# Kernel optimization log

Measured on AMD Instinct MI355X. Metric: run time of the kernel, lower is better.

## Reference

```python
import jax, jax.numpy as jnp
import numpy as np

EPS = 1e-5

def rms_norm(x):
    # SimpleRMSNorm (no learned weight), as used inside BitLinear158
    return x * jax.lax.rsqrt(jnp.mean(x * x, axis=-1, keepdims=True) + EPS)

def act_quant(x):
    # int8 absmax quantization per last-dim row, with straight-through estimator
    scale = 127.0 / jnp.clip(jnp.max(jnp.abs(x), axis=-1, keepdims=True), 1e-5)
    q = jnp.clip(jnp.round(x * scale), -128.0, 127.0) / scale
    return x + jax.lax.stop_gradient(q - x)

def weight_quant(w):
    # ternary {-1,0,1} absmean quantization, with straight-through estimator
    scale = 1.0 / jnp.clip(jnp.mean(jnp.abs(w)), 1e-5)
    q = jnp.clip(jnp.round(w * scale), -1.0, 1.0) / scale
    return w + jax.lax.stop_gradient(q - w)

def bitlinear158(x, w, b):
    xq = act_quant(rms_norm(x))          # [b,s,d_in]
    wq = weight_quant(w)                 # [d_out,d_in]
    return jnp.einsum('bsd,od->bso', xq, wq) + b

def layer_norm(x, g, b):
    mu = jnp.mean(x, axis=-1, keepdims=True)
    var = jnp.mean((x - mu) ** 2, axis=-1, keepdims=True)
    return (x - mu) * jax.lax.rsqrt(var + EPS) * g + b

def setup_inputs() -> dict:
    key = jax.random.key(0)
    ks = jax.random.split(key, 3)
    d, inner = 2048, 8192
    x = jax.random.normal(ks[0], (4, 2048, d), dtype=jnp.float32)
    w1 = jax.random.normal(ks[1], (inner, d), dtype=jnp.float32) * 0.02
    b1 = jnp.zeros((inner,), jnp.float32)
    ln_g = jnp.ones((inner,), jnp.float32)
    ln_b = jnp.zeros((inner,), jnp.float32)
    w2 = jax.random.normal(ks[2], (d, inner), dtype=jnp.float32) * 0.02
    b2 = jnp.zeros((d,), jnp.float32)
    return {"x": x, "w1": w1, "b1": b1, "ln_g": ln_g, "ln_b": ln_b, "w2": w2, "b2": b2}

def reference(x, w1, b1, ln_g, ln_b, w2, b2):
    h = jax.nn.silu(bitlinear158(x, w1, b1))        # project_in: BitLinear158 + SiLU
    h = jax.nn.gelu(h, approximate=False)            # nn.GELU (exact erf form)
    h = layer_norm(h, ln_g, ln_b)                    # nn.LayerNorm(inner_dim)
    return bitlinear158(h, w2, b2)                   # BitLinear158 out projection
```

## Files before the change

### kernel.cpp

```cpp
#include <hip/hip_runtime.h>
#include <hip/hip_bf16.h>
#include <math.h>

typedef __bf16 bf16_t;
typedef __bf16 bf16x4 __attribute__((ext_vector_type(4)));
typedef int i32x4 __attribute__((ext_vector_type(4)));

#define AS1 __attribute__((address_space(1)))
#define AS3 __attribute__((address_space(3)))

__device__ __forceinline__ void gl_lds16(const char* g, char* l) {
  __builtin_amdgcn_global_load_lds((const AS1 void*)g, (AS3 void*)l, 16, 0, 0);
}

__device__ __forceinline__ unsigned pack4i(float a, float b, float c, float d) {
  return ((unsigned)(unsigned char)(int)a) | ((unsigned)(unsigned char)(int)b << 8) |
         ((unsigned)(unsigned char)(int)c << 16) | ((unsigned)(unsigned char)(int)d << 24);
}

__device__ __forceinline__ float block_sum_f(float v) {
  __shared__ float sb[4];
  #pragma unroll
  for (int o = 32; o; o >>= 1) v += __shfl_xor(v, o);
  if ((threadIdx.x & 63) == 0) sb[threadIdx.x >> 6] = v;
  __syncthreads();
  v = sb[0] + sb[1] + sb[2] + sb[3];
  __syncthreads();
  return v;
}
__device__ __forceinline__ float block_max_f(float v) {
  __shared__ float sm[4];
  #pragma unroll
  for (int o = 32; o; o >>= 1) v = fmaxf(v, __shfl_xor(v, o));
  if ((threadIdx.x & 63) == 0) sm[threadIdx.x >> 6] = v;
  __syncthreads();
  v = fmaxf(fmaxf(sm[0], sm[1]), fmaxf(sm[2], sm[3]));
  __syncthreads();
  return v;
}

__global__ __launch_bounds__(256) void wabs_partial(const float* __restrict__ w, int n4,
                                                    double* __restrict__ part) {
  const float4* w4 = (const float4*)w;
  double s = 0.0;
  const int stride = gridDim.x * blockDim.x;
  for (int i = blockIdx.x * blockDim.x + threadIdx.x; i < n4; i += stride) {
    float4 v = w4[i];
    s += (double)fabsf(v.x) + (double)fabsf(v.y) + (double)fabsf(v.z) + (double)fabsf(v.w);
  }
  #pragma unroll
  for (int o = 32; o; o >>= 1) s += __shfl_xor(s, o);
  __shared__ double sd[4];
  if ((threadIdx.x & 63) == 0) sd[threadIdx.x >> 6] = s;
  __syncthreads();
  if (threadIdx.x == 0) part[blockIdx.x] = sd[0] + sd[1] + sd[2] + sd[3];
}

__global__ __launch_bounds__(256) void wabs_final(const double* __restrict__ part, int np,
                                                  double n, float* __restrict__ fwout) {
  double s = 0.0;
  for (int i = threadIdx.x; i < np; i += blockDim.x) s += part[i];
  #pragma unroll
  for (int o = 32; o; o >>= 1) s += __shfl_xor(s, o);
  __shared__ double sd[4];
  if ((threadIdx.x & 63) == 0) sd[threadIdx.x >> 6] = s;
  __syncthreads();
  if (threadIdx.x == 0) {
    double mean = (sd[0] + sd[1] + sd[2] + sd[3]) / n;
    fwout[0] = (float)fmax(mean, 1e-5);
  }
}

__global__ __launch_bounds__(256) void quant_w(const float* __restrict__ w,
                                               const float* __restrict__ fw,
                                               char* __restrict__ wq, int n4) {
  int i = blockIdx.x * blockDim.x + threadIdx.x;
  if (i >= n4) return;
  const float s = 1.0f / fw[0];
  float4 v = ((const float4*)w)[i];
  ((unsigned*)wq)[i] = pack4i(fminf(fmaxf(rintf(v.x * s), -1.f), 1.f),
                              fminf(fmaxf(rintf(v.y * s), -1.f), 1.f),
                              fminf(fmaxf(rintf(v.z * s), -1.f), 1.f),
                              fminf(fmaxf(rintf(v.w * s), -1.f), 1.f));
}

__global__ __launch_bounds__(256) void rms_quant_x(const float* __restrict__ x,
                                                   char* __restrict__ xq,
                                                   float* __restrict__ fx, int K) {
  const int row = blockIdx.x, t = threadIdx.x;
  const size_t base = (size_t)row * K;
  float v[8];
  float ss = 0.f;
  #pragma unroll
  for (int j = 0; j < 2; j++) {
    float4 lv = *(const float4*)(x + base + j * 1024 + t * 4);
    v[j*4+0] = lv.x; v[j*4+1] = lv.y; v[j*4+2] = lv.z; v[j*4+3] = lv.w;
  }
  #pragma unroll
  for (int i = 0; i < 8; i++) ss += v[i] * v[i];
  ss = block_sum_f(ss);
  const float r = 1.0f / sqrtf(ss / (float)K + 1e-5f);
  float amax = 0.f;
  #pragma unroll
  for (int i = 0; i < 8; i++) { v[i] *= r; amax = fmaxf(amax, fabsf(v[i])); }
  amax = block_max_f(amax);
  amax = fmaxf(amax, 1e-5f);
  const float scale = 127.0f / amax;
  #pragma unroll
  for (int j = 0; j < 2; j++) {
    float q[4];
    #pragma unroll
    for (int e = 0; e < 4; e++)
      q[e] = fminf(fmaxf(rintf(v[j*4+e] * scale), -128.f), 127.f);
    *(unsigned*)(xq + base + j * 1024 + t * 4) = pack4i(q[0], q[1], q[2], q[3]);
  }
  if (t == 0) fx[row] = amax / 127.0f;
}

__global__ __launch_bounds__(256) void ln_rms_quant(const bf16_t* __restrict__ h,
                                                    char* __restrict__ hq,
                                                    const float* __restrict__ g,
                                                    const float* __restrict__ bb,
                                                    float* __restrict__ fh, int N) {
  const int row = blockIdx.x, t = threadIdx.x;
  const size_t base = (size_t)row * N;
  float v[32];
  float s = 0.f, ss = 0.f;
  #pragma unroll
  for (int j = 0; j < 8; j++) {
    const int col = j * 1024 + t * 4;
    bf16x4 q = *(const bf16x4*)(h + base + col);
    v[j*4+0] = (float)q[0]; v[j*4+1] = (float)q[1];
    v[j*4+2] = (float)q[2]; v[j*4+3] = (float)q[3];
  }
  #pragma unroll
  for (int i = 0; i < 32; i++) { s += v[i]; ss += v[i] * v[i]; }
  s = block_sum_f(s);
  ss = block_sum_f(ss);
  const float mu = s / (float)N;
  const float var = ss / (float)N - mu * mu;
  const float rstd = 1.0f / sqrtf(var + 1e-5f);
  float ss2 = 0.f;
  #pragma unroll
  for (int j = 0; j < 8; j++) {
    const int col = j * 1024 + t * 4;
    float4 gv = *(const float4*)(g + col);
    float4 bv = *(const float4*)(bb + col);
    float y0 = (v[j*4+0] - mu) * rstd * gv.x + bv.x;
    float y1 = (v[j*4+1] - mu) * rstd * gv.y + bv.y;
    float y2 = (v[j*4+2] - mu) * rstd * gv.z + bv.z;
    float y3 = (v[j*4+3] - mu) * rstd * gv.w + bv.w;
    v[j*4+0] = y0; v[j*4+1] = y1; v[j*4+2] = y2; v[j*4+3] = y3;
    ss2 += y0*y0 + y1*y1 + y2*y2 + y3*y3;
  }
  ss2 = block_sum_f(ss2);
  const float r2 = 1.0f / sqrtf(ss2 / (float)N + 1e-5f);
  float amax = 0.f;
  #pragma unroll
  for (int i = 0; i < 32; i++) { v[i] *= r2; amax = fmaxf(amax, fabsf(v[i])); }
  amax = block_max_f(amax);
  amax = fmaxf(amax, 1e-5f);
  const float scale = 127.0f / amax;
  #pragma unroll
  for (int j = 0; j < 8; j++) {
    const int col = j * 1024 + t * 4;
    float q[4];
    #pragma unroll
    for (int e = 0; e < 4; e++)
      q[e] = fminf(fmaxf(rintf(v[j*4+e] * scale), -128.f), 127.f);
    *(unsigned*)(hq + base + col) = pack4i(q[0], q[1], q[2], q[3]);
  }
  if (t == 0) fh[row] = amax / 127.0f;
}

template<int EPI, bool STORE_BF16>
__global__ __launch_bounds__(512, 2) void gemm256(const char* __restrict__ A,
                                                  const char* __restrict__ B,
                                                  const float* __restrict__ rowf,
                                                  const float* __restrict__ wf,
                                                  const float* __restrict__ bias,
                                                  float* __restrict__ Cf,
                                                  bf16_t* __restrict__ Cb,
                                                  int M, int N, int K) {
  __shared__ char smem[98304];

  const int ntile = N >> 8;
  const int cpx = gridDim.x >> 3;
  const int bid = blockIdx.x;
  const int xcd = bid & 7, local = bid >> 3;
  int wg;
  const int mrows = cpx / ntile;
  if (mrows * ntile == cpx && mrows > 0) {
    const int bm_l = local % mrows, bn_i = local / mrows;
    wg = (xcd * mrows + bm_l) * ntile + bn_i;
  } else {
    wg = xcd * cpx + local;
  }
  const int bm = wg / ntile, bn = wg % ntile;
  const int tm = bm << 8, tn = bn << 8;

  const int tid = threadIdx.x;
  const int w = tid >> 6, lane = tid & 63;
  const int wm = w >> 2, wn = w & 3;
  const int ln15 = lane & 15;

  const int srow = lane >> 2;
  const int scol = (((lane & 3) ^ ((lane >> 3) & 3)) << 4);
  const size_t KS = (size_t)K;
  const char* pAst = A + (size_t)(tm + w * 16 + srow) * KS + scol;
  const char* pBst = B + (size_t)(tn + w * 16 + srow) * KS + scol;
  const size_t r128 = (size_t)128 * KS;
  const int dW = w * 1024;

  const int foff = ln15 * 64 + ((((lane >> 4) ^ ((ln15 >> 1) & 3))) << 4);

  i32x4 acc[8][4] = {};
  const int NT = K >> 6;

#define SB __builtin_amdgcn_sched_barrier(0)
#define BAR { SB; __builtin_amdgcn_s_barrier(); SB; }
#define LGKM0 { asm volatile("s_waitcnt lgkmcnt(0)" ::: "memory"); SB; }
#define VM(n) asm volatile("s_waitcnt vmcnt(" #n ")" ::: "memory")
#define ST_A(bb, kt) { const size_t ko = (size_t)(kt) * 64;                  \
    gl_lds16(pAst + ko,        smem + (bb) * 32768 + dW);                    \
    gl_lds16(pAst + r128 + ko, smem + (bb) * 32768 + 8192 + dW); }
#define ST_B(bb, kt) { const size_t ko = (size_t)(kt) * 64;                  \
    gl_lds16(pBst + ko,        smem + (bb) * 32768 + 16384 + dW);            \
    gl_lds16(pBst + r128 + ko, smem + (bb) * 32768 + 16384 + 8192 + dW); }
#define MM(AF, BF, MB, NB)                                                   \
  _Pragma("unroll") for (int m4 = 0; m4 < 4; m4++)                           \
    _Pragma("unroll") for (int n2 = 0; n2 < 2; n2++)                         \
      acc[(MB)+m4][(NB)+n2] = __builtin_amdgcn_mfma_i32_16x16x64_i8(         \
          AF[m4], BF[n2], acc[(MB)+m4][(NB)+n2], 0, 0, 0);

  ST_A(0, 0); ST_B(0, 0);
  ST_A(1, 1); ST_B(1, 1);
  VM(4);
  BAR;

  int cur = 0;
  for (int t = 0; t < NT; ++t) {
    int s2 = cur + 2; if (s2 >= 3) s2 -= 3;
    const char* sA = smem + cur * 32768;
    const char* sB = sA + 16384;
    i32x4 afL[4], afH[4], bL[2], bH[2];
    #pragma unroll
    for (int n2 = 0; n2 < 2; n2++)
      bL[n2] = *(const i32x4*)(sB + (wn * 2 + n2) * 1024 + foff);
    #pragma unroll
    for (int m4 = 0; m4 < 4; m4++)
      afL[m4] = *(const i32x4*)(sA + (wm * 4 + m4) * 1024 + foff);
    #pragma unroll
    for (int n2 = 0; n2 < 2; n2++)
      bH[n2] = *(const i32x4*)(sB + 8192 + (wn * 2 + n2) * 1024 + foff);
    if (t + 2 < NT) ST_A(s2, t + 2);
    SB;
    BAR;
    LGKM0;
    __builtin_amdgcn_s_setprio(1);
    MM(afL, bL, 0, 0);
    MM(afL, bH, 0, 2);
    __builtin_amdgcn_s_setprio(0);
    BAR;
    #pragma unroll
    for (int m4 = 0; m4 < 4; m4++)
      afH[m4] = *(const i32x4*)(sA + 8192 + (wm * 4 + m4) * 1024 + foff);
    if (t + 2 < NT) { ST_B(s2, t + 2); VM(4); }
    else if (t + 1 < NT) { VM(0); }
    SB;
    BAR;
    LGKM0;
    __builtin_amdgcn_s_setprio(1);
    MM(afH, bH, 4, 2);
    MM(afH, bL, 4, 0);
    __builtin_amdgcn_s_setprio(0);
    BAR;
    cur = cur + 1 == 3 ? 0 : cur + 1;
  }
#undef ST_A
#undef ST_B
#undef MM
#undef VM

  const float fwv = wf[0];
  const int rq = (lane >> 4) << 2;
  float rsc[8][4];
  #pragma unroll
  for (int m = 0; m < 8; m++)
    #pragma unroll
    for (int r = 0; r < 4; r++)
      rsc[m][r] = rowf[tm + (m >> 2) * 128 + wm * 64 + (m & 3) * 16 + rq + r] * fwv;

  #pragma unroll
  for (int m = 0; m < 8; m++) {
    #pragma unroll
    for (int n = 0; n < 4; n++) {
      const int col = tn + (n >> 1) * 128 + wn * 32 + (n & 1) * 16 + ln15;
      const float bv = bias[col];
      #pragma unroll
      for (int r = 0; r < 4; r++) {
        const int row = tm + (m >> 2) * 128 + wm * 64 + (m & 3) * 16 + rq + r;
        float val = (float)acc[m][n][r] * rsc[m][r] + bv;
        if (EPI == 1) {
          float sl = val / (1.0f + __expf(-val));
          val = 0.5f * sl * (1.0f + erff(sl * 0.70710678118654752f));
        }
        if (STORE_BF16) Cb[(size_t)row * N + col] = (bf16_t)val;
        else            Cf[(size_t)row * N + col] = val;
      }
    }
  }
}

extern "C" void kernel_launch(void* const* d_in, const int* in_sizes, int n_in,
                              void* d_out, int out_size, void* d_ws, size_t ws_size,
                              hipStream_t stream) {
  const float* x   = (const float*)d_in[0];
  const float* w1  = (const float*)d_in[1];
  const float* b1  = (const float*)d_in[2];
  const float* lng = (const float*)d_in[3];
  const float* lnb = (const float*)d_in[4];
  const float* w2  = (const float*)d_in[5];
  const float* b2  = (const float*)d_in[6];
  float* out = (float*)d_out;

  const int inner = in_sizes[2];
  const int d     = in_sizes[1] / inner;
  const int M     = in_sizes[0] / d;

  char* ws = (char*)d_ws;
  size_t off = 0;
  double* part = (double*)(ws + off); off += 1024 * 8;
  float*  fw   = (float*)(ws + off);  off += 256;
  float*  fx   = (float*)(ws + off);  off += (size_t)M * 4;
  float*  fh   = (float*)(ws + off);  off += (size_t)M * 4;
  char*   w1q  = ws + off;            off += (size_t)inner * d;
  char*   w2q  = ws + off;            off += (size_t)inner * d;

  int MC = M;
  while (MC > 256 && off + (size_t)MC * ((size_t)d + 3 * (size_t)inner) > ws_size) MC >>= 1;
  char*   xq = ws + off;              off += (size_t)MC * d;
  bf16_t* h  = (bf16_t*)(ws + off);   off += (size_t)MC * inner * 2;
  char*   hq = ws + off;

  const int nw = inner * d;
  const int n4 = nw / 4;

  wabs_partial<<<1024, 256, 0, stream>>>(w1, n4, part);
  wabs_final<<<1, 256, 0, stream>>>(part, 1024, (double)nw, fw + 0);
  wabs_partial<<<1024, 256, 0, stream>>>(w2, n4, part);
  wabs_final<<<1, 256, 0, stream>>>(part, 1024, (double)nw, fw + 1);
  quant_w<<<n4 / 256, 256, 0, stream>>>(w1, fw + 0, w1q, n4);
  quant_w<<<n4 / 256, 256, 0, stream>>>(w2, fw + 1, w2q, n4);

  for (int mc = 0; mc < M; mc += MC) {
    rms_quant_x<<<MC, 256, 0, stream>>>(x + (size_t)mc * d, xq, fx, d);

    const int g1 = (MC / 256) * (inner / 256);
    gemm256<1, true><<<g1, 512, 0, stream>>>(xq, w1q, fx, fw + 0, b1,
                                             nullptr, h, MC, inner, d);

    ln_rms_quant<<<MC, 256, 0, stream>>>(h, hq, lng, lnb, fh, inner);

    const int g2 = (MC / 256) * (d / 256);
    gemm256<0, false><<<g2, 512, 0, stream>>>(hq, w2q, fh, fw + 1, b2,
                                              out + (size_t)mc * d, nullptr, MC, d, inner);
  }
}
```

Before: 453.6 us.

## Register double-buffer LDS fragments with 4-stage LDS ring in int8 GEMM

Restructures the int8 MFMA GEMM main loop so each iteration issues both A and B global-to-LDS loads two tiles ahead into a 4-slot LDS ring. The next tile's LDS fragments are read into a second register set while the current tile's MFMAs run. This cuts the per-iteration barriers from four to one and removes the explicit lgkmcnt waits, aiming to overlap LDS reads with matrix math. In exchange, LDS grows to 128KB per block, which can halve occupancy under launch_bounds(512,2), and register pressure roughly doubles for fragments. It also assumes NT is even and relies on the compiler to insert correct LDS waits.

```diff
diff --git a/kernel.cpp b/kernel.cpp
--- a/kernel.cpp
+++ b/kernel.cpp
@@ -182,7 +182,7 @@
                                                   float* __restrict__ Cf,
                                                   bf16_t* __restrict__ Cb,
                                                   int M, int N, int K) {
-  __shared__ char smem[98304];
+  __shared__ char smem[131072];
 
   const int ntile = N >> 8;
   const int cpx = gridDim.x >> 3;
@@ -219,7 +219,6 @@
 
 #define SB __builtin_amdgcn_sched_barrier(0)
 #define BAR { SB; __builtin_amdgcn_s_barrier(); SB; }
-#define LGKM0 { asm volatile("s_waitcnt lgkmcnt(0)" ::: "memory"); SB; }
 #define VM(n) asm volatile("s_waitcnt vmcnt(" #n ")" ::: "memory")
 #define ST_A(bb, kt) { const size_t ko = (size_t)(kt) * 64;                  \
     gl_lds16(pAst + ko,        smem + (bb) * 32768 + dW);                    \
@@ -232,51 +231,57 @@
     _Pragma("unroll") for (int n2 = 0; n2 < 2; n2++)                         \
       acc[(MB)+m4][(NB)+n2] = __builtin_amdgcn_mfma_i32_16x16x64_i8(         \
           AF[m4], BF[n2], acc[(MB)+m4][(NB)+n2], 0, 0, 0);
+#define READ_AFL(AFL, bA) { _Pragma("unroll") for (int m4 = 0; m4 < 4; m4++) \
+    AFL[m4] = *(const i32x4*)((bA) + (wm * 4 + m4) * 1024 + foff); }
+#define READ_REST(AFH, BL, BH, bA, bB) {                                     \
+    _Pragma("unroll") for (int n2 = 0; n2 < 2; n2++)                         \
+      BL[n2] = *(const i32x4*)((bB) + (wn * 2 + n2) * 1024 + foff);          \
+    _Pragma("unroll") for (int n2 = 0; n2 < 2; n2++)                         \
+      BH[n2] = *(const i32x4*)((bB) + 8192 + (wn * 2 + n2) * 1024 + foff);   \
+    _Pragma("unroll") for (int m4 = 0; m4 < 4; m4++)                         \
+      AFH[m4] = *(const i32x4*)((bA) + 8192 + (wm * 4 + m4) * 1024 + foff); }
+
+#define ITER(T, MAFL, MBL, MBH, MAFH, FAFL, FBL, FBH, FAFH)                  \
+  { const int t_ = (T);                                                      \
+    if (t_ + 2 < NT) { const int sb_ = (t_ + 2) & 3;                         \
+      ST_A(sb_, t_ + 2); ST_B(sb_, t_ + 2); VM(4); }                         \
+    else if (t_ + 1 < NT) { VM(0); }                                         \
+    BAR;                                                                     \
+    const char* nA = smem + (size_t)((t_ + 1) & 3) * 32768;                  \
+    const char* nB = nA + 16384;                                             \
+    if (t_ + 1 < NT) READ_AFL(FAFL, nA);                                     \
+    SB;                                                                      \
+    __builtin_amdgcn_s_setprio(1);                                           \
+    MM(MAFL, MBL, 0, 0); MM(MAFL, MBH, 0, 2);                                \
+    __builtin_amdgcn_s_setprio(0);                                           \
+    SB;                                                                      \
+    if (t_ + 1 < NT) READ_REST(FAFH, FBL, FBH, nA, nB);                      \
+    SB;                                                                      \
+    __builtin_amdgcn_s_setprio(1);                                           \
+    MM(MAFH, MBH, 4, 2); MM(MAFH, MBL, 4, 0);                                \
+    __builtin_amdgcn_s_setprio(0);                                           \
+  }
 
   ST_A(0, 0); ST_B(0, 0);
   ST_A(1, 1); ST_B(1, 1);
   VM(4);
   BAR;
-
-  int cur = 0;
-  for (int t = 0; t < NT; ++t) {
-    int s2 = cur + 2; if (s2 >= 3) s2 -= 3;
-    const char* sA = smem + cur * 32768;
-    const char* sB = sA + 16384;
-    i32x4 afL[4], afH[4], bL[2], bH[2];
-    #pragma unroll
-    for (int n2 = 0; n2 < 2; n2++)
-      bL[n2] = *(const i32x4*)(sB + (wn * 2 + n2) * 1024 + foff);
-    #pragma unroll
-    for (int m4 = 0; m4 < 4; m4++)
-      afL[m4] = *(const i32x4*)(sA + (wm * 4 + m4) * 1024 + foff);
-    #pragma unroll
-    for (int n2 = 0; n2 < 2; n2++)
-      bH[n2] = *(const i32x4*)(sB + 8192 + (wn * 2 + n2) * 1024 + foff);
-    if (t + 2 < NT) ST_A(s2, t + 2);
-    SB;
-    BAR;
-    LGKM0;
-    __builtin_amdgcn_s_setprio(1);
-    MM(afL, bL, 0, 0);
-    MM(afL, bH, 0, 2);
-    __builtin_amdgcn_s_setprio(0);
-    BAR;
-    #pragma unroll
-    for (int m4 = 0; m4 < 4; m4++)
-      afH[m4] = *(const i32x4*)(sA + 8192 + (wm * 4 + m4) * 1024 + foff);
-    if (t + 2 < NT) { ST_B(s2, t + 2); VM(4); }
-    else if (t + 1 < NT) { VM(0); }
-    SB;
-    BAR;
-    LGKM0;
-    __builtin_amdgcn_s_setprio(1);
-    MM(afH, bH, 4, 2);
-    MM(afH, bL, 4, 0);
-    __builtin_amdgcn_s_setprio(0);
-    BAR;
-    cur = cur + 1 == 3 ? 0 : cur + 1;
-  }
+  i32x4 afL_A[4], afH_A[4], bL_A[2], bH_A[2];
+  i32x4 afL_B[4], afH_B[4], bL_B[2], bH_B[2];
+  {
+    const char* cA = smem;
+    const char* cB = smem + 16384;
+    READ_AFL(afL_A, cA);
+    READ_REST(afH_A, bL_A, bH_A, cA, cB);
+  }
+
+  for (int t = 0; t < NT; t += 2) {
+    ITER(t,     afL_A, bL_A, bH_A, afH_A,  afL_B, bL_B, bH_B, afH_B);
+    ITER(t + 1, afL_B, bL_B, bH_B, afH_B,  afL_A, bL_A, bH_A, afH_A);
+  }
+#undef ITER
+#undef READ_AFL
+#undef READ_REST
 #undef ST_A
 #undef ST_B
 #undef MM
```

Result: no change. 452.1 us (-0.3%).
